# Performance work log

Measured on AMD Instinct MI355X. Metric: run time of the kernel, lower is better.

Reference implementation:

```python
import jax, jax.numpy as jnp
import numpy as np

N_PTS = 500000
IN_DIM = 2
M_FOURIER = 32
J_WAVELET = 3
Q = 12
DEGREE = 3
N_CONTROL = 25
EMB_DIM = 2 * M_FOURIER + 2 * (2 ** J_WAVELET - 1)  # 78
LN_EPS = 1e-5


def make_open_uniform_knots(num_control, degree):
    n_knots = num_control + degree + 1  # 29
    if n_knots <= 2 * (degree + 1):
        return np.linspace(0.0, 1.0, n_knots).astype(np.float32)
    n_internal = n_knots - 2 * (degree + 1)
    internal = np.linspace(0.0, 1.0, n_internal + 2)[1:-1]
    return np.concatenate([np.zeros(degree + 1), internal, np.ones(degree + 1)]).astype(np.float32)

KNOTS = jnp.asarray(make_open_uniform_knots(N_CONTROL, DEGREE))


def bspline_basis(x, knots, degree, n_basis):
    # x: (M,) -> (M, n_basis); faithful (truncated) Cox-de-Boor as in source
    x = jnp.clip(x, knots[0], knots[-1])
    left = knots[:n_basis]
    right = knots[1:n_basis + 1]
    N = ((x[:, None] >= left) & (x[:, None] < right)).astype(x.dtype)
    last = ((x >= left[-1]) & (x <= right[-1])).astype(x.dtype)
    N = N.at[:, -1].set(last)
    for p in range(1, degree + 1):
        d1 = knots[p:p + n_basis] - knots[:n_basis]
        d2 = knots[p + 1:p + 1 + n_basis] - knots[1:1 + n_basis]
        c1 = jnp.where(d1 != 0, (x[:, None] - knots[:n_basis]) / jnp.where(d1 != 0, d1, 1.0), 0.0)
        c2 = jnp.where(d2 != 0, (knots[p + 1:p + 1 + n_basis] - x[:, None]) / jnp.where(d2 != 0, d2, 1.0), 0.0)
        N_shift = jnp.concatenate([N[:, 1:], jnp.zeros_like(N[:, :1])], axis=1)  # i+1 < n_basis guard
        N = c1 * N + c2 * N_shift
    return N


def wavelet_features_2d(z, J):
    x, t = z[:, 0], z[:, 1]
    feats = []
    for j in range(J):
        num_k = 2 ** j
        scale = max(0.5 / num_k, 0.001)
        centers = jnp.asarray([(k + 0.5) / num_k for k in range(num_k)], dtype=z.dtype)
        ux = x[:, None] - centers[None, :]
        ut = t[:, None] - centers[None, :]
        for u in (ux, ut):
            v = u / scale
            feats.append((1.0 - v * v) * jnp.exp(-0.5 * v * v))
    return jnp.concatenate(feats, axis=1)  # (N, 2*(2^J-1))


def setup_inputs() -> dict:
    key = jax.random.key(0)
    ks = jax.random.split(key, 6)
    xt = jax.random.uniform(ks[0], (N_PTS, IN_DIM), dtype=jnp.float32)
    B_fourier = jax.random.normal(ks[1], (M_FOURIER, IN_DIM), dtype=jnp.float32) * 1.0  # sigma_B
    ln_gamma = jnp.ones((EMB_DIM,), jnp.float32)
    ln_beta = jnp.zeros((EMB_DIM,), jnp.float32)
    W = jax.random.normal(ks[2], (Q, EMB_DIM), dtype=jnp.float32) * 0.05
    b_inner = jnp.zeros((Q,), jnp.float32)
    inner_scale = jnp.asarray(0.5, jnp.float32)
    coeffs = jax.random.normal(ks[3], (Q, N_CONTROL), dtype=jnp.float32) * 0.05
    a = jax.random.normal(ks[4], (Q, 1), dtype=jnp.float32) * 0.05
    b_out = jnp.zeros((1,), jnp.float32)
    return {"xt": xt, "B_fourier": B_fourier, "ln_gamma": ln_gamma, "ln_beta": ln_beta,
            "W": W, "b_inner": b_inner, "inner_scale": inner_scale, "coeffs": coeffs,
            "a": a, "b_out": b_out}


def reference(xt, B_fourier, ln_gamma, ln_beta, W, b_inner, inner_scale, coeffs, a, b_out):
    # Fourier features
    proj = (2.0 * np.pi) * (xt @ B_fourier.T)  # (N, M)
    scale = 1.0 / (np.sqrt(M_FOURIER) + 1e-12)
    F = jnp.concatenate([jnp.sin(proj) * scale, jnp.cos(proj) * scale], axis=1)
    # Wavelet features
    Wf = wavelet_features_2d(xt, J_WAVELET)
    emb = jnp.concatenate([F, Wf], axis=1)  # (N, 78)
    # LayerNorm
    mu = jnp.mean(emb, axis=-1, keepdims=True)
    var = jnp.mean(jnp.square(emb - mu), axis=-1, keepdims=True)
    emb = (emb - mu) / jnp.sqrt(var + LN_EPS) * ln_gamma + ln_beta
    # KAN B-spline core
    u_inner = emb @ W.T + b_inner  # (N, Q)
    s = 0.5 * (jnp.tanh(inner_scale * u_inner) + 1.0)
    B_flat = bspline_basis(s.reshape(-1), KNOTS, DEGREE, N_CONTROL)  # (N*Q, 25)
    B = B_flat.reshape(emb.shape[0], Q, N_CONTROL)
    phi = jnp.einsum('nqc,qc->nq', B, coeffs)
    u_out = phi @ a + b_out  # (N, 1)
    return u_out
```

## Files before the change

kernel.cpp:

```cpp
#include <hip/hip_runtime.h>
#include <hip/hip_bf16.h>
#include <math.h>

#define MF 32
#define EMB 78
#define NQ 12
#define NC 25
#define NSPAN 22
#define BLK 256
#define FSCALE 0.17677669529663688f

typedef __attribute__((ext_vector_type(8))) short short8;
typedef __attribute__((ext_vector_type(4))) float f32x4;

#define WS_A    0
#define WS_SGSB 768
#define WS_P    800

__device__ __forceinline__ float fast_rcp(float x) { return __builtin_amdgcn_rcpf(x); }
__device__ __forceinline__ float satf(float x) { return fminf(fmaxf(x, 0.0f), 1.0f); }

__device__ __forceinline__ unsigned pack2(float a, float b) {
    __hip_bfloat16 ha = __float2bfloat16(a), hb = __float2bfloat16(b);
    unsigned short ua, ub;
    __builtin_memcpy(&ua, &ha, 2); __builtin_memcpy(&ub, &hb, 2);
    return (unsigned)ua | ((unsigned)ub << 16);
}

__device__ __forceinline__ float4 deboor4(float s, int ii) {
    const float c22 = 1.0f / 22.0f;
    float k_m2 = satf((float)(ii - 2) * c22);
    float k_m1 = satf((float)(ii - 1) * c22);
    float k_0  = satf((float)(ii)     * c22);
    float k_p1 = satf((float)(ii + 1) * c22);
    float k_p2 = satf((float)(ii + 2) * c22);
    float k_p3 = satf((float)(ii + 3) * c22);
    float l1 = s - k_0, l2 = s - k_m1, l3 = s - k_m2;
    float r1 = k_p1 - s, r2 = k_p2 - s, r3 = k_p3 - s;
    float t0 = fast_rcp(r1 + l1);
    float N0 = r1 * t0, N1 = l1 * t0;
    float ta = N0 * fast_rcp(r1 + l2);
    float tb = N1 * fast_rcp(r2 + l1);
    N0 = r1 * ta;
    N1 = fmaf(l2, ta, r2 * tb);
    float N2 = l1 * tb;
    float tc = N0 * fast_rcp(r1 + l3);
    float td = N1 * fast_rcp(r2 + l2);
    float te = N2 * fast_rcp(r3 + l1);
    N0 = r1 * tc;
    N1 = fmaf(l3, tc, r2 * td);
    N2 = fmaf(l2, td, r3 * te);
    float N3 = l1 * te;
    return make_float4(N0, N1, N2, N3);
}

__device__ __forceinline__ float wgf(const float* g, const float* W, int q, int k) {
    if (q >= NQ || k >= EMB) return 0.0f;
    float v = g[k] * W[q * EMB + k];
    return (k < 2 * MF) ? v * FSCALE : v;
}

__global__ __launch_bounds__(256) void pikan_setup(
    const float* __restrict__ g, const float* __restrict__ be,
    const float* __restrict__ W, const float* __restrict__ bi,
    const float* __restrict__ coeffs, const float* __restrict__ a,
    float* __restrict__ ws)
{
    const int tid = threadIdx.x;
    unsigned* wsu = (unsigned*)ws;

    for (int i = tid; i < 768; i += 256) {
        int d = i & 3, l = (i >> 2) & 63, kt = i >> 8;
        int q = l & 15;
        int kb = kt * 32 + (l >> 4) * 8 + d * 2;
        wsu[WS_A + i] = pack2(wgf(g, W, q, kb), wgf(g, W, q, kb + 1));
    }
    if (tid < 16) {
        float sg = 0.f, sb = 0.f;
        if (tid < NQ) {
            for (int e = 0; e < EMB; ++e) {
                float w = W[tid * EMB + e];
                sg += g[e] * w;
                sb += be[e] * w;
            }
            sb += bi[tid];
        }
        ws[WS_SGSB + 2 * tid]     = sg;
        ws[WS_SGSB + 2 * tid + 1] = sb;
    }
    for (int i = tid; i < 16 * NSPAN; i += 256) {
        int q = i / NSPAN, ii = i - q * NSPAN;
        float4 o = make_float4(0.f, 0.f, 0.f, 0.f);
        if (q < NQ) {
            float f[4];
            #pragma unroll
            for (int j = 0; j < 4; ++j) {
                float u = (float)j / 3.0f;
                float s = ((float)ii + u) * (1.0f / 22.0f);
                float4 N = deboor4(s, ii);
                const float* cq = coeffs + q * NC + ii;
                f[j] = N.x * cq[0] + N.y * cq[1] + N.z * cq[2] + N.w * cq[3];
            }
            float c0 = f[0];
            float c1 = -5.5f * f[0] +  9.0f * f[1] -  4.5f * f[2] +  1.0f * f[3];
            float c2 =  9.0f * f[0] - 22.5f * f[1] + 18.0f * f[2] -  4.5f * f[3];
            float c3 = -4.5f * f[0] + 13.5f * f[1] - 13.5f * f[2] +  4.5f * f[3];
            float aq = a[q];
            o = make_float4(c0 * aq, c1 * aq, c2 * aq, c3 * aq);
        }
        reinterpret_cast<float4*>(ws + WS_P)[i] = o;
    }
}

__global__ __launch_bounds__(BLK, 4) void pikan_main(
    const float* __restrict__ xt, const float* __restrict__ Bf,
    const float* __restrict__ isc_p, const float* __restrict__ bout_p,
    const float* __restrict__ ws, float* __restrict__ out, int npts)
{
    __shared__ uint4  sEmb[4][256];
    __shared__ float4 sPoly[16 * NSPAN];

    const int tid = threadIdx.x;
    for (int i = tid; i < 16 * NSPAN; i += BLK)
        sPoly[i] = reinterpret_cast<const float4*>(ws + WS_P)[i];
    __syncthreads();

    const int l = tid & 63, w = tid >> 6;
    const int g16 = l >> 4, c16 = l & 15;
    const int sw = (l >> 1) & 3;
    uint4* myEmb = sEmb[w];

    float sgq[4], sbq[4];
    #pragma unroll
    for (int r = 0; r < 4; ++r) {
        int q = g16 * 4 + r;
        sgq[r] = ws[WS_SGSB + 2 * q];
        sbq[r] = ws[WS_SGSB + 2 * q + 1];
    }
    const float kexp = -2.0f * isc_p[0] * 1.4426950408889634f;
    const float bout = bout_p[0];
    const int base = (blockIdx.x * 4 + w) * 128;

    #pragma unroll 1
    for (int pass = 0; pass < 2; ++pass) {
        const int pbase = base + pass * 64;
        const int pt = pbase + l;
        const bool valid = pt < npts;
        float x = 0.f, t = 0.f;
        if (valid) { float2 p = reinterpret_cast<const float2*>(xt)[pt]; x = p.x; t = p.y; }

        f32x4 acc[4];
        #pragma unroll
        for (int n = 0; n < 4; ++n) acc[n] = (f32x4){0.f, 0.f, 0.f, 0.f};

        auto stage = [&](uint4 a0, uint4 a1, uint4 a2, uint4 a3) {
            myEmb[l * 4 + (0 ^ sw)] = a0;
            myEmb[l * 4 + (1 ^ sw)] = a1;
            myEmb[l * 4 + (2 ^ sw)] = a2;
            myEmb[l * 4 + (3 ^ sw)] = a3;
        };
        auto mfma_kt = [&](int kt) {
            uint4 au = reinterpret_cast<const uint4*>(ws)[kt * 64 + l];
            short8 af = __builtin_bit_cast(short8, au);
            #pragma unroll
            for (int n = 0; n < 4; ++n) {
                int p = n * 16 + c16;
                uint4 bu = myEmb[p * 4 + (g16 ^ sw)];
                short8 bf = __builtin_bit_cast(short8, bu);
                acc[n] = __builtin_amdgcn_mfma_f32_16x16x32_bf16(af, bf, acc[n], 0, 0, 0);
            }
        };

        float sumf = 0.f, ssf = 0.f;
        unsigned spk[16], cpk[16];
        #pragma unroll
        for (int mp = 0; mp < 16; ++mp) {
            float rev0 = fmaf(x, Bf[4 * mp + 0], t * Bf[4 * mp + 1]);
            float rev1 = fmaf(x, Bf[4 * mp + 2], t * Bf[4 * mp + 3]);
#if __has_builtin(__builtin_amdgcn_fractf)
            float f0 = __builtin_amdgcn_fractf(rev0);
            float f1 = __builtin_amdgcn_fractf(rev1);
#else
            float f0 = rev0 - floorf(rev0);
            float f1 = rev1 - floorf(rev1);
#endif
            float s0 = __builtin_amdgcn_sinf(f0), s1 = __builtin_amdgcn_sinf(f1);
            float c0 = __builtin_amdgcn_cosf(f0), c1 = __builtin_amdgcn_cosf(f1);
            sumf += (s0 + s1) + (c0 + c1);
            ssf = fmaf(s0, s0, fmaf(s1, s1, fmaf(c0, c0, fmaf(c1, c1, ssf))));
            spk[mp] = pack2(s0, s1);
            cpk[mp] = pack2(c0, c1);
        }
        stage(make_uint4(spk[0], spk[1], spk[2],  spk[3]),
              make_uint4(spk[4], spk[5], spk[6],  spk[7]),
              make_uint4(spk[8], spk[9], spk[10], spk[11]),
              make_uint4(spk[12], spk[13], spk[14], spk[15]));
        mfma_kt(0);
        stage(make_uint4(cpk[0], cpk[1], cpk[2],  cpk[3]),
              make_uint4(cpk[4], cpk[5], cpk[6],  cpk[7]),
              make_uint4(cpk[8], cpk[9], cpk[10], cpk[11]),
              make_uint4(cpk[12], cpk[13], cpk[14], cpk[15]));
        mfma_kt(1);

        float w14[14];
        float sumw = 0.f, ssw = 0.f;
        {
            int o = 0;
            #pragma unroll
            for (int j = 0; j < 3; ++j) {
                const int nk = 1 << j;
                const float inv = (float)(2 * nk);
                #pragma unroll
                for (int k = 0; k < nk; ++k) {
                    float c = ((float)k + 0.5f) / (float)nk;
                    float v = (x - c) * inv, v2 = v * v;
                    float f = (1.0f - v2) * __expf(-0.5f * v2);
                    w14[o + k] = f; sumw += f; ssw = fmaf(f, f, ssw);
                }
                #pragma unroll
                for (int k = 0; k < nk; ++k) {
                    float c = ((float)k + 0.5f) / (float)nk;
                    float v = (t - c) * inv, v2 = v * v;
                    float f = (1.0f - v2) * __expf(-0.5f * v2);
                    w14[o + nk + k] = f; sumw += f; ssw = fmaf(f, f, ssw);
                }
                o += 2 * nk;
            }
        }
        stage(make_uint4(pack2(w14[0], w14[1]), pack2(w14[2], w14[3]),
                         pack2(w14[4], w14[5]), pack2(w14[6], w14[7])),
              make_uint4(pack2(w14[8], w14[9]), pack2(w14[10], w14[11]),
                         pack2(w14[12], w14[13]), 0u),
              make_uint4(0u, 0u, 0u, 0u),
              make_uint4(0u, 0u, 0u, 0u));
        mfma_kt(2);

        const float sum = fmaf(FSCALE, sumf, sumw);
        const float ssq = fmaf(FSCALE * FSCALE, ssf, ssw);
        const float mu = sum * (1.0f / EMB);
        float var = fmaf(-mu, mu, ssq * (1.0f / EMB));
        var = fmaxf(var, 0.0f);
        const float istd = rsqrtf(var + 1e-5f);

        float yout = 0.f;
        #pragma unroll
        for (int n = 0; n < 4; ++n) {
            float mun  = __shfl(mu,   n * 16 + c16);
            float istn = __shfl(istd, n * 16 + c16);
            float yn = 0.f;
            #pragma unroll
            for (int r = 0; r < 4; ++r) {
                float uq = fmaf(istn, fmaf(-mun, sgq[r], acc[n][r]), sbq[r]);
                float e2 = __builtin_amdgcn_exp2f(kexp * uq);
                float s = fast_rcp(1.0f + e2);
                float v = s * 22.0f;
                int ii = (int)v; ii = ii > 21 ? 21 : ii;
                float uu = v - (float)ii;
                float4 cc = sPoly[(g16 * 4 + r) * NSPAN + ii];
                yn += fmaf(fmaf(fmaf(cc.w, uu, cc.z), uu, cc.y), uu, cc.x);
            }
            yn += __shfl_xor(yn, 16);
            yn += __shfl_xor(yn, 32);
            if (g16 == n) yout = yn;
        }
        if (valid) out[pt] = yout + bout;
    }
}

extern "C" void kernel_launch(void* const* d_in, const int* in_sizes, int n_in,
                              void* d_out, int out_size, void* d_ws, size_t ws_size,
                              hipStream_t stream) {
    const float* xt          = (const float*)d_in[0];
    const float* Bf          = (const float*)d_in[1];
    const float* gamma       = (const float*)d_in[2];
    const float* beta        = (const float*)d_in[3];
    const float* W           = (const float*)d_in[4];
    const float* b_inner     = (const float*)d_in[5];
    const float* inner_scale = (const float*)d_in[6];
    const float* coeffs      = (const float*)d_in[7];
    const float* a           = (const float*)d_in[8];
    const float* b_out       = (const float*)d_in[9];
    float* out = (float*)d_out;
    float* ws  = (float*)d_ws;

    const int npts = in_sizes[0] / 2;
    pikan_setup<<<1, 256, 0, stream>>>(gamma, beta, W, b_inner, coeffs, a, ws);
    const int grid = (npts + 511) / 512;
    pikan_main<<<grid, BLK, 0, stream>>>(xt, Bf, inner_scale, b_out, ws, out, npts);
}
```

Baseline: 25.15 us.

## Build MFMA weight fragments in-kernel, replicate spline table in LDS, prefetch points

The setup kernel now only builds the per-span cubic polynomial table and uses two blocks. The main kernel builds its bf16 W·gamma MFMA A-fragments and the gamma/beta projection sums directly from W, gamma and beta in registers, using wave shuffles, instead of reading them from workspace. The spline polynomial table is replicated four times in LDS, indexed by lane, to reduce bank conflicts on the data-dependent lookups. Both passes' input points are loaded up front. In exchange, every block redoes the fragment construction, LDS usage grows, and register pressure rises from holding three fragments.

```diff
diff --git a/kernel.cpp b/kernel.cpp
--- a/kernel.cpp
+++ b/kernel.cpp
@@ -13,10 +13,6 @@
 typedef __attribute__((ext_vector_type(8))) short short8;
 typedef __attribute__((ext_vector_type(4))) float f32x4;
 
-#define WS_A    0
-#define WS_SGSB 768
-#define WS_P    800
-
 __device__ __forceinline__ float fast_rcp(float x) { return __builtin_amdgcn_rcpf(x); }
 __device__ __forceinline__ float satf(float x) { return fminf(fmaxf(x, 0.0f), 1.0f); }
 
@@ -25,6 +21,12 @@
     unsigned short ua, ub;
     __builtin_memcpy(&ua, &ha, 2); __builtin_memcpy(&ub, &hb, 2);
     return (unsigned)ua | ((unsigned)ub << 16);
+}
+__device__ __forceinline__ float upk_lo(unsigned u) {
+    unsigned v = u << 16; float f; __builtin_memcpy(&f, &v, 4); return f;
+}
+__device__ __forceinline__ float upk_hi(unsigned u) {
+    unsigned v = u & 0xffff0000u; float f; __builtin_memcpy(&f, &v, 4); return f;
 }
 
 __device__ __forceinline__ float4 deboor4(float s, int ii) {
@@ -54,100 +56,134 @@
     return make_float4(N0, N1, N2, N3);
 }
 
-__device__ __forceinline__ float wgf(const float* g, const float* W, int q, int k) {
-    if (q >= NQ || k >= EMB) return 0.0f;
-    float v = g[k] * W[q * EMB + k];
-    return (k < 2 * MF) ? v * FSCALE : v;
-}
-
 __global__ __launch_bounds__(256) void pikan_setup(
-    const float* __restrict__ g, const float* __restrict__ be,
-    const float* __restrict__ W, const float* __restrict__ bi,
     const float* __restrict__ coeffs, const float* __restrict__ a,
     float* __restrict__ ws)
 {
-    const int tid = threadIdx.x;
-    unsigned* wsu = (unsigned*)ws;
-
-    for (int i = tid; i < 768; i += 256) {
-        int d = i & 3, l = (i >> 2) & 63, kt = i >> 8;
-        int q = l & 15;
-        int kb = kt * 32 + (l >> 4) * 8 + d * 2;
-        wsu[WS_A + i] = pack2(wgf(g, W, q, kb), wgf(g, W, q, kb + 1));
-    }
-    if (tid < 16) {
-        float sg = 0.f, sb = 0.f;
-        if (tid < NQ) {
-            for (int e = 0; e < EMB; ++e) {
-                float w = W[tid * EMB + e];
-                sg += g[e] * w;
-                sb += be[e] * w;
-            }
-            sb += bi[tid];
-        }
-        ws[WS_SGSB + 2 * tid]     = sg;
-        ws[WS_SGSB + 2 * tid + 1] = sb;
-    }
-    for (int i = tid; i < 16 * NSPAN; i += 256) {
-        int q = i / NSPAN, ii = i - q * NSPAN;
-        float4 o = make_float4(0.f, 0.f, 0.f, 0.f);
-        if (q < NQ) {
-            float f[4];
-            #pragma unroll
-            for (int j = 0; j < 4; ++j) {
-                float u = (float)j / 3.0f;
-                float s = ((float)ii + u) * (1.0f / 22.0f);
-                float4 N = deboor4(s, ii);
-                const float* cq = coeffs + q * NC + ii;
-                f[j] = N.x * cq[0] + N.y * cq[1] + N.z * cq[2] + N.w * cq[3];
-            }
-            float c0 = f[0];
-            float c1 = -5.5f * f[0] +  9.0f * f[1] -  4.5f * f[2] +  1.0f * f[3];
-            float c2 =  9.0f * f[0] - 22.5f * f[1] + 18.0f * f[2] -  4.5f * f[3];
-            float c3 = -4.5f * f[0] + 13.5f * f[1] - 13.5f * f[2] +  4.5f * f[3];
-            float aq = a[q];
-            o = make_float4(c0 * aq, c1 * aq, c2 * aq, c3 * aq);
-        }
-        reinterpret_cast<float4*>(ws + WS_P)[i] = o;
-    }
+    int i = blockIdx.x * 256 + threadIdx.x;
+    if (i >= 16 * NSPAN) return;
+    int q = i / NSPAN, ii = i - q * NSPAN;
+    float4 o = make_float4(0.f, 0.f, 0.f, 0.f);
+    if (q < NQ) {
+        float f[4];
+        #pragma unroll
+        for (int j = 0; j < 4; ++j) {
+            float u = (float)j / 3.0f;
+            float s = ((float)ii + u) * (1.0f / 22.0f);
+            float4 N = deboor4(s, ii);
+            const float* cq = coeffs + q * NC + ii;
+            f[j] = N.x * cq[0] + N.y * cq[1] + N.z * cq[2] + N.w * cq[3];
+        }
+        float c0 = f[0];
+        float c1 = -5.5f * f[0] +  9.0f * f[1] -  4.5f * f[2] +  1.0f * f[3];
+        float c2 =  9.0f * f[0] - 22.5f * f[1] + 18.0f * f[2] -  4.5f * f[3];
+        float c3 = -4.5f * f[0] + 13.5f * f[1] - 13.5f * f[2] +  4.5f * f[3];
+        float aq = a[q];
+        o = make_float4(c0 * aq, c1 * aq, c2 * aq, c3 * aq);
+    }
+    reinterpret_cast<float4*>(ws)[i] = o;
 }
 
 __global__ __launch_bounds__(BLK, 4) void pikan_main(
     const float* __restrict__ xt, const float* __restrict__ Bf,
+    const float* __restrict__ g, const float* __restrict__ be,
+    const float* __restrict__ W, const float* __restrict__ bi,
     const float* __restrict__ isc_p, const float* __restrict__ bout_p,
-    const float* __restrict__ ws, float* __restrict__ out, int npts)
+    const float* __restrict__ wsP, float* __restrict__ out, int npts)
 {
     __shared__ uint4  sEmb[4][256];
-    __shared__ float4 sPoly[16 * NSPAN];
+    __shared__ float4 sPoly[4][16 * NSPAN + 1];
 
     const int tid = threadIdx.x;
-    for (int i = tid; i < 16 * NSPAN; i += BLK)
-        sPoly[i] = reinterpret_cast<const float4*>(ws + WS_P)[i];
+    for (int i = tid; i < 16 * NSPAN; i += BLK) {
+        float4 v = reinterpret_cast<const float4*>(wsP)[i];
+        sPoly[0][i] = v; sPoly[1][i] = v; sPoly[2][i] = v; sPoly[3][i] = v;
+    }
     __syncthreads();
 
     const int l = tid & 63, w = tid >> 6;
     const int g16 = l >> 4, c16 = l & 15;
     const int sw = (l >> 1) & 3;
     uint4* myEmb = sEmb[w];
-
+    const float4* myPoly = sPoly[l & 3];
+
+    const bool qok = c16 < NQ;
+    uint4 afrag[3];
+    float sgF = 0.f, sgW = 0.f, sbp = 0.f;
+    #pragma unroll
+    for (int kt = 0; kt < 2; ++kt) {
+        const int k0 = kt * 32 + g16 * 8;
+        float wr[8];
+        #pragma unroll
+        for (int h = 0; h < 4; ++h) {
+            float2 wv = make_float2(0.f, 0.f);
+            if (qok) wv = *reinterpret_cast<const float2*>(W + c16 * EMB + k0 + 2 * h);
+            wr[2 * h] = wv.x; wr[2 * h + 1] = wv.y;
+        }
+        float4 ga = *reinterpret_cast<const float4*>(g + k0);
+        float4 gb = *reinterpret_cast<const float4*>(g + k0 + 4);
+        float4 ba = *reinterpret_cast<const float4*>(be + k0);
+        float4 bb = *reinterpret_cast<const float4*>(be + k0 + 4);
+        float gv[8] = {ga.x, ga.y, ga.z, ga.w, gb.x, gb.y, gb.z, gb.w};
+        float bv[8] = {ba.x, ba.y, ba.z, ba.w, bb.x, bb.y, bb.z, bb.w};
+        unsigned dw[4];
+        #pragma unroll
+        for (int d = 0; d < 4; ++d) {
+            float v0 = gv[2 * d]     * wr[2 * d]     * FSCALE;
+            float v1 = gv[2 * d + 1] * wr[2 * d + 1] * FSCALE;
+            dw[d] = pack2(v0, v1);
+            sgF += upk_lo(dw[d]) + upk_hi(dw[d]);
+            sbp = fmaf(bv[2 * d], wr[2 * d], fmaf(bv[2 * d + 1], wr[2 * d + 1], sbp));
+        }
+        afrag[kt] = make_uint4(dw[0], dw[1], dw[2], dw[3]);
+    }
+    {
+        float v[8];
+        #pragma unroll
+        for (int j = 0; j < 8; ++j) {
+            int k = 64 + g16 * 8 + j;
+            bool ok = qok && (k < EMB);
+            float wr = ok ? W[c16 * EMB + k] : 0.f;
+            float gk = ok ? g[k] : 0.f;
+            float bk = ok ? be[k] : 0.f;
+            v[j] = gk * wr;
+            sbp = fmaf(bk, wr, sbp);
+        }
+        unsigned dw[4];
+        #pragma unroll
+        for (int d = 0; d < 4; ++d) {
+            dw[d] = pack2(v[2 * d], v[2 * d + 1]);
+            sgW += upk_lo(dw[d]) + upk_hi(dw[d]);
+        }
+        afrag[2] = make_uint4(dw[0], dw[1], dw[2], dw[3]);
+    }
+    float sg = fmaf(sgF, 1.0f / FSCALE, sgW);
+    sg += __shfl_xor(sg, 16); sg += __shfl_xor(sg, 32);
+    float sb = sbp;
+    sb += __shfl_xor(sb, 16); sb += __shfl_xor(sb, 32);
+    sb += qok ? bi[c16] : 0.f;
     float sgq[4], sbq[4];
     #pragma unroll
     for (int r = 0; r < 4; ++r) {
-        int q = g16 * 4 + r;
-        sgq[r] = ws[WS_SGSB + 2 * q];
-        sbq[r] = ws[WS_SGSB + 2 * q + 1];
-    }
+        sgq[r] = __shfl(sg, g16 * 4 + r);
+        sbq[r] = __shfl(sb, g16 * 4 + r);
+    }
+
     const float kexp = -2.0f * isc_p[0] * 1.4426950408889634f;
     const float bout = bout_p[0];
     const int base = (blockIdx.x * 4 + w) * 128;
 
+    const int pt0 = base + l, pt1 = base + 64 + l;
+    float2 p0 = make_float2(0.f, 0.f), p1 = make_float2(0.f, 0.f);
+    if (pt0 < npts) p0 = reinterpret_cast<const float2*>(xt)[pt0];
+    if (pt1 < npts) p1 = reinterpret_cast<const float2*>(xt)[pt1];
+
     #pragma unroll 1
     for (int pass = 0; pass < 2; ++pass) {
-        const int pbase = base + pass * 64;
-        const int pt = pbase + l;
+        const int pt = pass ? pt1 : pt0;
         const bool valid = pt < npts;
-        float x = 0.f, t = 0.f;
-        if (valid) { float2 p = reinterpret_cast<const float2*>(xt)[pt]; x = p.x; t = p.y; }
+        const float x = pass ? p1.x : p0.x;
+        const float t = pass ? p1.y : p0.y;
 
         f32x4 acc[4];
         #pragma unroll
@@ -159,8 +195,7 @@
             myEmb[l * 4 + (2 ^ sw)] = a2;
             myEmb[l * 4 + (3 ^ sw)] = a3;
         };
-        auto mfma_kt = [&](int kt) {
-            uint4 au = reinterpret_cast<const uint4*>(ws)[kt * 64 + l];
+        auto mfma_kt = [&](uint4 au) {
             short8 af = __builtin_bit_cast(short8, au);
             #pragma unroll
             for (int n = 0; n < 4; ++n) {
@@ -195,12 +230,12 @@
               make_uint4(spk[4], spk[5], spk[6],  spk[7]),
               make_uint4(spk[8], spk[9], spk[10], spk[11]),
               make_uint4(spk[12], spk[13], spk[14], spk[15]));
-        mfma_kt(0);
+        mfma_kt(afrag[0]);
         stage(make_uint4(cpk[0], cpk[1], cpk[2],  cpk[3]),
               make_uint4(cpk[4], cpk[5], cpk[6],  cpk[7]),
               make_uint4(cpk[8], cpk[9], cpk[10], cpk[11]),
               make_uint4(cpk[12], cpk[13], cpk[14], cpk[15]));
-        mfma_kt(1);
+        mfma_kt(afrag[1]);
 
         float w14[14];
         float sumw = 0.f, ssw = 0.f;
@@ -233,7 +268,7 @@
                          pack2(w14[12], w14[13]), 0u),
               make_uint4(0u, 0u, 0u, 0u),
               make_uint4(0u, 0u, 0u, 0u));
-        mfma_kt(2);
+        mfma_kt(afrag[2]);
 
         const float sum = fmaf(FSCALE, sumf, sumw);
         const float ssq = fmaf(FSCALE * FSCALE, ssf, ssw);
@@ -256,7 +291,7 @@
                 float v = s * 22.0f;
                 int ii = (int)v; ii = ii > 21 ? 21 : ii;
                 float uu = v - (float)ii;
-                float4 cc = sPoly[(g16 * 4 + r) * NSPAN + ii];
+                float4 cc = myPoly[(g16 * 4 + r) * NSPAN + ii];
                 yn += fmaf(fmaf(fmaf(cc.w, uu, cc.z), uu, cc.y), uu, cc.x);
             }
             yn += __shfl_xor(yn, 16);
@@ -284,7 +319,8 @@
     float* ws  = (float*)d_ws;
 
     const int npts = in_sizes[0] / 2;
-    pikan_setup<<<1, 256, 0, stream>>>(gamma, beta, W, b_inner, coeffs, a, ws);
+    pikan_setup<<<2, 256, 0, stream>>>(coeffs, a, ws);
     const int grid = (npts + 511) / 512;
-    pikan_main<<<grid, BLK, 0, stream>>>(xt, Bf, inner_scale, b_out, ws, out, npts);
-}
+    pikan_main<<<grid, BLK, 0, stream>>>(xt, Bf, gamma, beta, W, b_inner,
+                                         inner_scale, b_out, ws, out, npts);
+}
```

Result: slower. 31.79 us (+26.4%).

## Compute embedding directly in MFMA B-operand layout, drop LDS staging

Applied to the files above, without the earlier changes.

Each lane now computes only the 8 Fourier sin/cos pairs and 8 wavelet features that belong to its slot of the MFMA B fragment, for the point it owns in each 16-column group. This removes the LDS round-trip for embeddings and the redundant per-lane computation of all 78 features. LayerNorm statistics are then reduced across lanes with shuffles. The A fragments and xt loads are hoisted out of the pass loop, and the polynomial table is replicated four times in LDS to reduce bank conflicts on lookups. The cost is more shuffles and a larger LDS footprint for the table.

```diff
diff --git a/kernel.cpp b/kernel.cpp
--- a/kernel.cpp
+++ b/kernel.cpp
@@ -117,18 +117,22 @@
     const float* __restrict__ isc_p, const float* __restrict__ bout_p,
     const float* __restrict__ ws, float* __restrict__ out, int npts)
 {
-    __shared__ uint4  sEmb[4][256];
-    __shared__ float4 sPoly[16 * NSPAN];
+    __shared__ float4 sPoly[4][16 * NSPAN + 1];
 
     const int tid = threadIdx.x;
-    for (int i = tid; i < 16 * NSPAN; i += BLK)
-        sPoly[i] = reinterpret_cast<const float4*>(ws + WS_P)[i];
+    for (int i = tid; i < 16 * NSPAN; i += BLK) {
+        float4 v = reinterpret_cast<const float4*>(ws + WS_P)[i];
+        sPoly[0][i] = v; sPoly[1][i] = v; sPoly[2][i] = v; sPoly[3][i] = v;
+    }
     __syncthreads();
 
     const int l = tid & 63, w = tid >> 6;
     const int g16 = l >> 4, c16 = l & 15;
-    const int sw = (l >> 1) & 3;
-    uint4* myEmb = sEmb[w];
+    const float4* myPoly = sPoly[l & 3];
+
+    const uint4 af0 = reinterpret_cast<const uint4*>(ws)[0 * 64 + l];
+    const uint4 af1 = reinterpret_cast<const uint4*>(ws)[1 * 64 + l];
+    const uint4 af2 = reinterpret_cast<const uint4*>(ws)[2 * 64 + l];
 
     float sgq[4], sbq[4];
     #pragma unroll
@@ -137,133 +141,130 @@
         sgq[r] = ws[WS_SGSB + 2 * q];
         sbq[r] = ws[WS_SGSB + 2 * q + 1];
     }
+
+    float4 bf4[4];
+    #pragma unroll
+    for (int h = 0; h < 4; ++h)
+        bf4[h] = reinterpret_cast<const float4*>(Bf)[g16 * 4 + h];
+
+    float selj[8], cij[8], ivj[8];
+    #pragma unroll
+    for (int j = 0; j < 8; ++j) {
+        int wi = g16 * 8 + j;
+        int lvl = (wi < 2) ? 0 : (wi < 6) ? 1 : 2;
+        int nk = 1 << lvl;
+        int r = wi - 2 * (nk - 1);
+        bool isx = r < nk;
+        int kk = isx ? r : r - nk;
+        float inv = (float)(2 * nk);
+        float c = ((float)kk + 0.5f) / (float)nk;
+        bool ok = (wi < 14);
+        selj[j] = isx ? 1.0f : 0.0f;
+        ivj[j]  = ok ? inv : 0.0f;
+        cij[j]  = ok ? (c * inv) : -100.0f;
+    }
+
     const float kexp = -2.0f * isc_p[0] * 1.4426950408889634f;
     const float bout = bout_p[0];
     const int base = (blockIdx.x * 4 + w) * 128;
 
-    #pragma unroll 1
+    float2 cA[4], cB[4];
+    #pragma unroll
+    for (int n = 0; n < 4; ++n) {
+        int pa = base + n * 16 + c16;
+        int pb = base + 64 + n * 16 + c16;
+        cA[n] = (pa < npts) ? reinterpret_cast<const float2*>(xt)[pa] : make_float2(0.f, 0.f);
+        cB[n] = (pb < npts) ? reinterpret_cast<const float2*>(xt)[pb] : make_float2(0.f, 0.f);
+    }
+
+    #pragma unroll
     for (int pass = 0; pass < 2; ++pass) {
         const int pbase = base + pass * 64;
-        const int pt = pbase + l;
-        const bool valid = pt < npts;
-        float x = 0.f, t = 0.f;
-        if (valid) { float2 p = reinterpret_cast<const float2*>(xt)[pt]; x = p.x; t = p.y; }
-
-        f32x4 acc[4];
-        #pragma unroll
-        for (int n = 0; n < 4; ++n) acc[n] = (f32x4){0.f, 0.f, 0.f, 0.f};
-
-        auto stage = [&](uint4 a0, uint4 a1, uint4 a2, uint4 a3) {
-            myEmb[l * 4 + (0 ^ sw)] = a0;
-            myEmb[l * 4 + (1 ^ sw)] = a1;
-            myEmb[l * 4 + (2 ^ sw)] = a2;
-            myEmb[l * 4 + (3 ^ sw)] = a3;
-        };
-        auto mfma_kt = [&](int kt) {
-            uint4 au = reinterpret_cast<const uint4*>(ws)[kt * 64 + l];
-            short8 af = __builtin_bit_cast(short8, au);
-            #pragma unroll
-            for (int n = 0; n < 4; ++n) {
-                int p = n * 16 + c16;
-                uint4 bu = myEmb[p * 4 + (g16 ^ sw)];
-                short8 bf = __builtin_bit_cast(short8, bu);
-                acc[n] = __builtin_amdgcn_mfma_f32_16x16x32_bf16(af, bf, acc[n], 0, 0, 0);
-            }
-        };
-
-        float sumf = 0.f, ssf = 0.f;
-        unsigned spk[16], cpk[16];
-        #pragma unroll
-        for (int mp = 0; mp < 16; ++mp) {
-            float rev0 = fmaf(x, Bf[4 * mp + 0], t * Bf[4 * mp + 1]);
-            float rev1 = fmaf(x, Bf[4 * mp + 2], t * Bf[4 * mp + 3]);
-#if __has_builtin(__builtin_amdgcn_fractf)
-            float f0 = __builtin_amdgcn_fractf(rev0);
-            float f1 = __builtin_amdgcn_fractf(rev1);
-#else
-            float f0 = rev0 - floorf(rev0);
-            float f1 = rev1 - floorf(rev1);
-#endif
-            float s0 = __builtin_amdgcn_sinf(f0), s1 = __builtin_amdgcn_sinf(f1);
-            float c0 = __builtin_amdgcn_cosf(f0), c1 = __builtin_amdgcn_cosf(f1);
-            sumf += (s0 + s1) + (c0 + c1);
-            ssf = fmaf(s0, s0, fmaf(s1, s1, fmaf(c0, c0, fmaf(c1, c1, ssf))));
-            spk[mp] = pack2(s0, s1);
-            cpk[mp] = pack2(c0, c1);
-        }
-        stage(make_uint4(spk[0], spk[1], spk[2],  spk[3]),
-              make_uint4(spk[4], spk[5], spk[6],  spk[7]),
-              make_uint4(spk[8], spk[9], spk[10], spk[11]),
-              make_uint4(spk[12], spk[13], spk[14], spk[15]));
-        mfma_kt(0);
-        stage(make_uint4(cpk[0], cpk[1], cpk[2],  cpk[3]),
-              make_uint4(cpk[4], cpk[5], cpk[6],  cpk[7]),
-              make_uint4(cpk[8], cpk[9], cpk[10], cpk[11]),
-              make_uint4(cpk[12], cpk[13], cpk[14], cpk[15]));
-        mfma_kt(1);
-
-        float w14[14];
-        float sumw = 0.f, ssw = 0.f;
-        {
-            int o = 0;
-            #pragma unroll
-            for (int j = 0; j < 3; ++j) {
-                const int nk = 1 << j;
-                const float inv = (float)(2 * nk);
-                #pragma unroll
-                for (int k = 0; k < nk; ++k) {
-                    float c = ((float)k + 0.5f) / (float)nk;
-                    float v = (x - c) * inv, v2 = v * v;
-                    float f = (1.0f - v2) * __expf(-0.5f * v2);
-                    w14[o + k] = f; sumw += f; ssw = fmaf(f, f, ssw);
-                }
-                #pragma unroll
-                for (int k = 0; k < nk; ++k) {
-                    float c = ((float)k + 0.5f) / (float)nk;
-                    float v = (t - c) * inv, v2 = v * v;
-                    float f = (1.0f - v2) * __expf(-0.5f * v2);
-                    w14[o + nk + k] = f; sumw += f; ssw = fmaf(f, f, ssw);
-                }
-                o += 2 * nk;
-            }
-        }
-        stage(make_uint4(pack2(w14[0], w14[1]), pack2(w14[2], w14[3]),
-                         pack2(w14[4], w14[5]), pack2(w14[6], w14[7])),
-              make_uint4(pack2(w14[8], w14[9]), pack2(w14[10], w14[11]),
-                         pack2(w14[12], w14[13]), 0u),
-              make_uint4(0u, 0u, 0u, 0u),
-              make_uint4(0u, 0u, 0u, 0u));
-        mfma_kt(2);
-
-        const float sum = fmaf(FSCALE, sumf, sumw);
-        const float ssq = fmaf(FSCALE * FSCALE, ssf, ssw);
-        const float mu = sum * (1.0f / EMB);
-        float var = fmaf(-mu, mu, ssq * (1.0f / EMB));
-        var = fmaxf(var, 0.0f);
-        const float istd = rsqrtf(var + 1e-5f);
-
         float yout = 0.f;
+
         #pragma unroll
         for (int n = 0; n < 4; ++n) {
-            float mun  = __shfl(mu,   n * 16 + c16);
-            float istn = __shfl(istd, n * 16 + c16);
+            const float xn = pass ? cB[n].x : cA[n].x;
+            const float tn = pass ? cB[n].y : cA[n].y;
+
+            float sv[8], cv[8];
+            #pragma unroll
+            for (int h = 0; h < 4; ++h) {
+                float rev0 = fmaf(xn, bf4[h].x, tn * bf4[h].y);
+                float rev1 = fmaf(xn, bf4[h].z, tn * bf4[h].w);
+#if __has_builtin(__builtin_amdgcn_fractf)
+                float f0 = __builtin_amdgcn_fractf(rev0);
+                float f1 = __builtin_amdgcn_fractf(rev1);
+#else
+                float f0 = rev0 - floorf(rev0);
+                float f1 = rev1 - floorf(rev1);
+#endif
+                sv[2 * h]     = __builtin_amdgcn_sinf(f0);
+                cv[2 * h]     = __builtin_amdgcn_cosf(f0);
+                sv[2 * h + 1] = __builtin_amdgcn_sinf(f1);
+                cv[2 * h + 1] = __builtin_amdgcn_cosf(f1);
+            }
+
+            float wv[8];
+            const float dxt = xn - tn;
+            #pragma unroll
+            for (int j = 0; j < 8; ++j) {
+                float bse = fmaf(selj[j], dxt, tn);
+                float v = fmaf(bse, ivj[j], -cij[j]);
+                float v2 = v * v;
+                wv[j] = (1.0f - v2) * __expf(-0.5f * v2);
+            }
+
+            float sF = 0.f, qF = 0.f, sW = 0.f, qW = 0.f;
+            #pragma unroll
+            for (int j = 0; j < 8; ++j) {
+                sF += sv[j] + cv[j];
+                qF = fmaf(sv[j], sv[j], fmaf(cv[j], cv[j], qF));
+                sW += wv[j];
+                qW = fmaf(wv[j], wv[j], qW);
+            }
+            float sm = fmaf(FSCALE, sF, sW);
+            float sq = fmaf(FSCALE * FSCALE, qF, qW);
+            sm += __shfl_xor(sm, 16); sm += __shfl_xor(sm, 32);
+            sq += __shfl_xor(sq, 16); sq += __shfl_xor(sq, 32);
+            const float mu = sm * (1.0f / EMB);
+            float var = fmaf(-mu, mu, sq * (1.0f / EMB));
+            var = fmaxf(var, 0.0f);
+            const float istd = rsqrtf(var + 1e-5f);
+
+            uint4 b0 = make_uint4(pack2(sv[0], sv[1]), pack2(sv[2], sv[3]),
+                                  pack2(sv[4], sv[5]), pack2(sv[6], sv[7]));
+            uint4 b1 = make_uint4(pack2(cv[0], cv[1]), pack2(cv[2], cv[3]),
+                                  pack2(cv[4], cv[5]), pack2(cv[6], cv[7]));
+            uint4 b2 = make_uint4(pack2(wv[0], wv[1]), pack2(wv[2], wv[3]),
+                                  pack2(wv[4], wv[5]), pack2(wv[6], wv[7]));
+            f32x4 acc = (f32x4){0.f, 0.f, 0.f, 0.f};
+            acc = __builtin_amdgcn_mfma_f32_16x16x32_bf16(
+                __builtin_bit_cast(short8, af0), __builtin_bit_cast(short8, b0), acc, 0, 0, 0);
+            acc = __builtin_amdgcn_mfma_f32_16x16x32_bf16(
+                __builtin_bit_cast(short8, af1), __builtin_bit_cast(short8, b1), acc, 0, 0, 0);
+            acc = __builtin_amdgcn_mfma_f32_16x16x32_bf16(
+                __builtin_bit_cast(short8, af2), __builtin_bit_cast(short8, b2), acc, 0, 0, 0);
+
             float yn = 0.f;
             #pragma unroll
             for (int r = 0; r < 4; ++r) {
-                float uq = fmaf(istn, fmaf(-mun, sgq[r], acc[n][r]), sbq[r]);
+                float uq = fmaf(istd, fmaf(-mu, sgq[r], acc[r]), sbq[r]);
                 float e2 = __builtin_amdgcn_exp2f(kexp * uq);
                 float s = fast_rcp(1.0f + e2);
-                float v = s * 22.0f;
-                int ii = (int)v; ii = ii > 21 ? 21 : ii;
-                float uu = v - (float)ii;
-                float4 cc = sPoly[(g16 * 4 + r) * NSPAN + ii];
+                float vv = s * 22.0f;
+                int ii = (int)vv; ii = ii > 21 ? 21 : ii;
+                float uu = vv - (float)ii;
+                float4 cc = myPoly[(g16 * 4 + r) * NSPAN + ii];
                 yn += fmaf(fmaf(fmaf(cc.w, uu, cc.z), uu, cc.y), uu, cc.x);
             }
             yn += __shfl_xor(yn, 16);
             yn += __shfl_xor(yn, 32);
             if (g16 == n) yout = yn;
         }
-        if (valid) out[pt] = yout + bout;
+
+        const int pt = pbase + l;
+        if (pt < npts) out[pt] = yout + bout;
     }
 }
 
```

After: 32.91 us. +30.8%, slower.

## Replicate spline LDS table, hoist weight and point loads, use sin²+cos² identity

Applied to the files above, without the earlier changes.

Keeps four copies of the spline polynomial table in shared memory and picks one per lane (l&3), which spreads the random gathers across banks to reduce bank conflicts. Hoists the three MFMA weight-fragment loads and both passes' point loads out of the pass loop. Replaces the per-feature Fourier sum of squares with the constant 32 (sin²+cos²=1), dropping 64 FMAs per point. The cost is four times the LDS for the table and a few more live registers.

```diff
diff --git a/kernel.cpp b/kernel.cpp
--- a/kernel.cpp
+++ b/kernel.cpp
@@ -118,17 +118,24 @@
     const float* __restrict__ ws, float* __restrict__ out, int npts)
 {
     __shared__ uint4  sEmb[4][256];
-    __shared__ float4 sPoly[16 * NSPAN];
+    __shared__ float4 sPoly[4][16 * NSPAN + 1];
 
     const int tid = threadIdx.x;
-    for (int i = tid; i < 16 * NSPAN; i += BLK)
-        sPoly[i] = reinterpret_cast<const float4*>(ws + WS_P)[i];
+    for (int i = tid; i < 16 * NSPAN; i += BLK) {
+        float4 v = reinterpret_cast<const float4*>(ws + WS_P)[i];
+        sPoly[0][i] = v; sPoly[1][i] = v; sPoly[2][i] = v; sPoly[3][i] = v;
+    }
     __syncthreads();
 
     const int l = tid & 63, w = tid >> 6;
     const int g16 = l >> 4, c16 = l & 15;
     const int sw = (l >> 1) & 3;
     uint4* myEmb = sEmb[w];
+    const float4* myPoly = sPoly[l & 3];
+
+    const uint4 af0 = reinterpret_cast<const uint4*>(ws)[0 * 64 + l];
+    const uint4 af1 = reinterpret_cast<const uint4*>(ws)[1 * 64 + l];
+    const uint4 af2 = reinterpret_cast<const uint4*>(ws)[2 * 64 + l];
 
     float sgq[4], sbq[4];
     #pragma unroll
@@ -137,17 +144,22 @@
         sgq[r] = ws[WS_SGSB + 2 * q];
         sbq[r] = ws[WS_SGSB + 2 * q + 1];
     }
+
     const float kexp = -2.0f * isc_p[0] * 1.4426950408889634f;
     const float bout = bout_p[0];
     const int base = (blockIdx.x * 4 + w) * 128;
 
+    const int pt0 = base + l, pt1 = base + 64 + l;
+    float2 p0 = make_float2(0.f, 0.f), p1 = make_float2(0.f, 0.f);
+    if (pt0 < npts) p0 = reinterpret_cast<const float2*>(xt)[pt0];
+    if (pt1 < npts) p1 = reinterpret_cast<const float2*>(xt)[pt1];
+
     #pragma unroll 1
     for (int pass = 0; pass < 2; ++pass) {
-        const int pbase = base + pass * 64;
-        const int pt = pbase + l;
+        const int pt = pass ? pt1 : pt0;
         const bool valid = pt < npts;
-        float x = 0.f, t = 0.f;
-        if (valid) { float2 p = reinterpret_cast<const float2*>(xt)[pt]; x = p.x; t = p.y; }
+        const float x = pass ? p1.x : p0.x;
+        const float t = pass ? p1.y : p0.y;
 
         f32x4 acc[4];
         #pragma unroll
@@ -159,8 +171,7 @@
             myEmb[l * 4 + (2 ^ sw)] = a2;
             myEmb[l * 4 + (3 ^ sw)] = a3;
         };
-        auto mfma_kt = [&](int kt) {
-            uint4 au = reinterpret_cast<const uint4*>(ws)[kt * 64 + l];
+        auto mfma_kt = [&](uint4 au) {
             short8 af = __builtin_bit_cast(short8, au);
             #pragma unroll
             for (int n = 0; n < 4; ++n) {
@@ -171,7 +182,7 @@
             }
         };
 
-        float sumf = 0.f, ssf = 0.f;
+        float sumf = 0.f;
         unsigned spk[16], cpk[16];
         #pragma unroll
         for (int mp = 0; mp < 16; ++mp) {
@@ -187,7 +198,6 @@
             float s0 = __builtin_amdgcn_sinf(f0), s1 = __builtin_amdgcn_sinf(f1);
             float c0 = __builtin_amdgcn_cosf(f0), c1 = __builtin_amdgcn_cosf(f1);
             sumf += (s0 + s1) + (c0 + c1);
-            ssf = fmaf(s0, s0, fmaf(s1, s1, fmaf(c0, c0, fmaf(c1, c1, ssf))));
             spk[mp] = pack2(s0, s1);
             cpk[mp] = pack2(c0, c1);
         }
@@ -195,12 +205,12 @@
               make_uint4(spk[4], spk[5], spk[6],  spk[7]),
               make_uint4(spk[8], spk[9], spk[10], spk[11]),
               make_uint4(spk[12], spk[13], spk[14], spk[15]));
-        mfma_kt(0);
+        mfma_kt(af0);
         stage(make_uint4(cpk[0], cpk[1], cpk[2],  cpk[3]),
               make_uint4(cpk[4], cpk[5], cpk[6],  cpk[7]),
               make_uint4(cpk[8], cpk[9], cpk[10], cpk[11]),
               make_uint4(cpk[12], cpk[13], cpk[14], cpk[15]));
-        mfma_kt(1);
+        mfma_kt(af1);
 
         float w14[14];
         float sumw = 0.f, ssw = 0.f;
@@ -233,10 +243,10 @@
                          pack2(w14[12], w14[13]), 0u),
               make_uint4(0u, 0u, 0u, 0u),
               make_uint4(0u, 0u, 0u, 0u));
-        mfma_kt(2);
+        mfma_kt(af2);
 
         const float sum = fmaf(FSCALE, sumf, sumw);
-        const float ssq = fmaf(FSCALE * FSCALE, ssf, ssw);
+        const float ssq = fmaf(FSCALE * FSCALE, 32.0f, ssw);
         const float mu = sum * (1.0f / EMB);
         float var = fmaf(-mu, mu, ssq * (1.0f / EMB));
         var = fmaxf(var, 0.0f);
@@ -256,7 +266,7 @@
                 float v = s * 22.0f;
                 int ii = (int)v; ii = ii > 21 ? 21 : ii;
                 float uu = v - (float)ii;
-                float4 cc = sPoly[(g16 * 4 + r) * NSPAN + ii];
+                float4 cc = myPoly[(g16 * 4 + r) * NSPAN + ii];
                 yn += fmaf(fmaf(fmaf(cc.w, uu, cc.z), uu, cc.y), uu, cc.x);
             }
             yn += __shfl_xor(yn, 16);
```

Result: slower. 26.90 us (+7.0%).
